# Kernel tuning notes

Measured on AMD Instinct MI355X. Metric: run time of the kernel, lower is better.

Reference implementation:

```python
import jax, jax.numpy as jnp
import numpy as np

D = 512          # input_size (feature dim)
C = 100          # num_classes
N = 2048         # test samples
ALPHA = 0.5      # regularization mixing parameter
SHRINK = 1e-4    # shrinkage_param


def setup_inputs() -> dict:
    key = jax.random.key(0)
    k1, k2, k3, k4, k5 = jax.random.split(key, 5)
    X = jax.random.normal(k1, (N, D), dtype=jnp.float32)
    muK = jax.random.normal(k2, (C, D), dtype=jnp.float32)
    # Per-class covariances: PSD, well-conditioned (like fitted streaming covariances)
    A = jax.random.normal(k3, (C, D, D), dtype=jnp.float32) * 0.05
    SigmaK = jnp.einsum('cij,ckj->cik', A, A) + 0.1 * jnp.eye(D, dtype=jnp.float32)
    B = jax.random.normal(k4, (D, D), dtype=jnp.float32) * 0.05
    Sigma = B @ B.T + 0.1 * jnp.eye(D, dtype=jnp.float32)
    # class counts (all > 0 so every class is active)
    cK = jax.random.uniform(k5, (C,), dtype=jnp.float32, minval=1.0, maxval=1000.0)
    return {"X": X, "muK": muK, "SigmaK": SigmaK, "Sigma": Sigma, "cK": cK}


def reference(X, muK, SigmaK, Sigma, cK):
    # RegSigmaK[k] = alpha * SigmaK[k] + (1-alpha) * Sigma           [C, D, D]
    RegSigmaK = ALPHA * SigmaK + (1.0 - ALPHA) * Sigma[None, :, :]
    # priors (classes with zero count get prior 1, then are masked to -inf below)
    s = jnp.sum(cK)
    prior = jnp.where(cK == 0, 1.0, cK / s)                          # [C]
    # Lambda[k] = pinv((1-sh) * RegSigmaK[k] + sh * I)               [C, D, D]
    eye = jnp.eye(D, dtype=RegSigmaK.dtype)
    Lambda = jnp.linalg.pinv((1.0 - SHRINK) * RegSigmaK + SHRINK * eye)
    # 0.5 * log ||RegSigmaK[k]||_F  (torch.norm default = Frobenius)
    half_lognorm = 0.5 * jnp.log(jnp.linalg.norm(RegSigmaK, axis=(1, 2)))  # [C]
    # batched Mahalanobis quadratic form: (x - mu_k)^T Lambda_k (x - mu_k)
    diff = X[:, None, :] - muK[None, :, :]                           # [N, C, D]
    quad = jnp.einsum('ncd,cde,nce->nc', diff, Lambda, diff)         # [N, C]
    scores = jnp.log(prior)[None, :] - half_lognorm[None, :] - 0.5 * quad
    scores = jnp.where((cK == 0)[None, :], -jnp.inf, scores)
    return scores
```

## Files before the change

kernel.cpp:

```cpp
#include <hip/hip_runtime.h>
#include <math.h>

#define DIM 512
#define NCLS 100
#define NS 2048
#define DD (DIM*DIM)
#define SHRINKV 1e-4f

typedef short bf16x8 __attribute__((ext_vector_type(8)));
typedef short s16x4 __attribute__((ext_vector_type(4)));
typedef float f32x4 __attribute__((ext_vector_type(4)));

static __device__ __forceinline__ short f2bf(float f) {
  unsigned int u = __float_as_uint(f);
  u += 0x7FFFu + ((u >> 16) & 1u);
  return (short)(u >> 16);
}

__global__ void aux_kernel(const float* __restrict__ cK, float* __restrict__ aux) {
  __shared__ float red[128];
  int t = threadIdx.x;
  float v = (t < NCLS) ? cK[t] : 0.f;
  if (t < NCLS) aux[1 + t] = 0.f;
  red[t] = v;
  __syncthreads();
  for (int o = 64; o > 0; o >>= 1) {
    if (t < o) red[t] += red[t + o];
    __syncthreads();
  }
  if (t == 0) aux[0] = red[0];
}

__global__ __launch_bounds__(256) void prep_kernel(const float* __restrict__ SigmaK,
                                                   const float* __restrict__ Sigma,
                                                   float* __restrict__ M,
                                                   float* __restrict__ aux) {
  int b = blockIdx.x;
  int k = b >> 2, chunk = b & 3;
  const float* Sk = SigmaK + (size_t)k * DD;
  float* Mk = M + (size_t)k * DD;
  int base0 = chunk << 16;
  float fro = 0.f;
  const float oms = 1.0f - SHRINKV;
  for (int it = 0; it < 64; ++it) {
    int idx = base0 + (it << 10) + (threadIdx.x << 2);
    float4 a = *(const float4*)(Sk + idx);
    float4 g = *(const float4*)(Sigma + idx);
    int r = idx >> 9, c = idx & 511;
    float4 reg;
    reg.x = 0.5f*(a.x + g.x); reg.y = 0.5f*(a.y + g.y);
    reg.z = 0.5f*(a.z + g.z); reg.w = 0.5f*(a.w + g.w);
    fro += reg.x*reg.x + reg.y*reg.y + reg.z*reg.z + reg.w*reg.w;
    float4 m;
    m.x = oms*reg.x + ((r == c + 0) ? SHRINKV : 0.f);
    m.y = oms*reg.y + ((r == c + 1) ? SHRINKV : 0.f);
    m.z = oms*reg.z + ((r == c + 2) ? SHRINKV : 0.f);
    m.w = oms*reg.w + ((r == c + 3) ? SHRINKV : 0.f);
    *(float4*)(Mk + idx) = m;
  }
  __shared__ float red[4];
  int lane = threadIdx.x & 63, w = threadIdx.x >> 6;
  for (int o = 32; o > 0; o >>= 1) fro += __shfl_down(fro, o);
  if (lane == 0) red[w] = fro;
  __syncthreads();
  if (threadIdx.x == 0) atomicAdd(&aux[1 + k], red[0] + red[1] + red[2] + red[3]);
}

__global__ __launch_bounds__(64) void fdiag_kernel(float* __restrict__ M,
                                                   short* __restrict__ Wb, int p) {
  __shared__ float Llds[64 * 68];
  int kcls = blockIdx.x;
  int lane = threadIdx.x;
  int p0 = p << 6;
  float* Mk = M + (size_t)kcls * DD;
  short* Wk = Wb + (size_t)kcls * DD;
  float row[64];
  {
    const float* src = Mk + (size_t)(p0 + lane) * DIM + p0;
    #pragma unroll
    for (int c4 = 0; c4 < 64; c4 += 4) {
      float4 v = *(const float4*)(src + c4);
      row[c4] = v.x; row[c4+1] = v.y; row[c4+2] = v.z; row[c4+3] = v.w;
    }
  }
  #pragma unroll
  for (int j = 0; j < 64; ++j) {
    float diagv = __shfl(row[j], j);
    float dv = sqrtf(diagv);
    float rinv = 1.0f / dv;
    float myLj = row[j] * rinv;
    row[j] = myLj;
    #pragma unroll
    for (int c = j + 1; c < 64; ++c)
      row[c] = fmaf(-myLj, __shfl(myLj, c), row[c]);
  }
  #pragma unroll
  for (int c = 0; c < 64; ++c)
    Llds[lane * 68 + c] = (c <= lane) ? row[c] : 0.f;
  __syncthreads();
  float w[64];
  #pragma unroll
  for (int r = 0; r < 64; ++r) {
    float s = 0.f;
    #pragma unroll
    for (int kk = 0; kk + 4 <= r; kk += 4) {
      float4 lv = *(const float4*)(Llds + r*68 + kk);
      s += lv.x*w[kk] + lv.y*w[kk+1] + lv.z*w[kk+2] + lv.w*w[kk+3];
    }
    #pragma unroll
    for (int kk = r & ~3; kk < r; ++kk) s += Llds[r*68 + kk] * w[kk];
    float rhs = ((r == lane) ? 1.0f : 0.0f) - s;
    w[r] = rhs / Llds[r*68 + r];
  }
  #pragma unroll
  for (int r = 0; r < 64; ++r) {
    Mk[(size_t)(p0 + r)*DIM + p0 + lane] = w[r];
    Wk[(size_t)(p0 + r)*DIM + p0 + lane] = f2bf(w[r]);
  }
}

__global__ __launch_bounds__(256) void trsm_kernel(float* __restrict__ M, int p) {
  __shared__ float TA[64 * 68];
  __shared__ float TB[64 * 68];
  int n = 7 - p;
  int cls = blockIdx.x / n;
  int bi = blockIdx.x % n;
  int i = p + 1 + bi;
  float* Mk = M + (size_t)cls * DD;
  int tid = threadIdx.x;
  int ty = tid >> 4, tx = tid & 15;
  int sr = tid >> 2, sq = (tid & 3) << 4;
  {
    const float* a = Mk + (size_t)((i << 6) + sr)*DIM + (p << 6) + sq;
    const float* b = Mk + (size_t)((p << 6) + sr)*DIM + (p << 6) + sq;
    #pragma unroll
    for (int t4 = 0; t4 < 4; ++t4) {
      float4 va = *(const float4*)(a + 4*t4);
      TA[(sq+4*t4+0)*68+sr]=va.x; TA[(sq+4*t4+1)*68+sr]=va.y;
      TA[(sq+4*t4+2)*68+sr]=va.z; TA[(sq+4*t4+3)*68+sr]=va.w;
      float4 vb = *(const float4*)(b + 4*t4);
      TB[(sq+4*t4+0)*68+sr]=vb.x; TB[(sq+4*t4+1)*68+sr]=vb.y;
      TB[(sq+4*t4+2)*68+sr]=vb.z; TB[(sq+4*t4+3)*68+sr]=vb.w;
    }
  }
  __syncthreads();
  float acc[4][4];
  #pragma unroll
  for (int a = 0; a < 4; ++a)
    #pragma unroll
    for (int b = 0; b < 4; ++b) acc[a][b] = 0.f;
  #pragma unroll 16
  for (int m = 0; m < 64; ++m) {
    float4 av = *(const float4*)(TA + m*68 + (ty << 2));
    float4 bv = *(const float4*)(TB + m*68 + (tx << 2));
    float a4[4] = {av.x, av.y, av.z, av.w};
    float b4[4] = {bv.x, bv.y, bv.z, bv.w};
    #pragma unroll
    for (int ir = 0; ir < 4; ++ir)
      #pragma unroll
      for (int ic = 0; ic < 4; ++ic) acc[ir][ic] += a4[ir] * b4[ic];
  }
  #pragma unroll
  for (int q = 0; q < 4; ++q) {
    float4 v; v.x = acc[q][0]; v.y = acc[q][1]; v.z = acc[q][2]; v.w = acc[q][3];
    *(float4*)(Mk + (size_t)((i << 6) + (ty << 2) + q)*DIM + (p << 6) + (tx << 2)) = v;
  }
}

__global__ __launch_bounds__(256) void syrk_kernel(float* __restrict__ M, int p) {
  __shared__ float TA[64 * 68];
  __shared__ float TB[64 * 68];
  int n = 7 - p;
  int T = n * (n + 1) / 2;
  int cls = blockIdx.x / T;
  int t = blockIdx.x % T;
  int bi = 0;
  while (t > bi) { t -= bi + 1; ++bi; }
  int i = p + 1 + bi, j = p + 1 + t;
  float* Mk = M + (size_t)cls * DD;
  int tid = threadIdx.x;
  int ty = tid >> 4, tx = tid & 15;
  int sr = tid >> 2, sq = (tid & 3) << 4;
  {
    const float* a = Mk + (size_t)((i << 6) + sr)*DIM + (p << 6) + sq;
    const float* b = Mk + (size_t)((j << 6) + sr)*DIM + (p << 6) + sq;
    #pragma unroll
    for (int t4 = 0; t4 < 4; ++t4) {
      float4 va = *(const float4*)(a + 4*t4);
      TA[(sq+4*t4+0)*68+sr]=va.x; TA[(sq+4*t4+1)*68+sr]=va.y;
      TA[(sq+4*t4+2)*68+sr]=va.z; TA[(sq+4*t4+3)*68+sr]=va.w;
      float4 vb = *(const float4*)(b + 4*t4);
      TB[(sq+4*t4+0)*68+sr]=vb.x; TB[(sq+4*t4+1)*68+sr]=vb.y;
      TB[(sq+4*t4+2)*68+sr]=vb.z; TB[(sq+4*t4+3)*68+sr]=vb.w;
    }
  }
  __syncthreads();
  float acc[4][4];
  #pragma unroll
  for (int a = 0; a < 4; ++a)
    #pragma unroll
    for (int b = 0; b < 4; ++b) acc[a][b] = 0.f;
  #pragma unroll 16
  for (int m = 0; m < 64; ++m) {
    float4 av = *(const float4*)(TA + m*68 + (ty << 2));
    float4 bv = *(const float4*)(TB + m*68 + (tx << 2));
    float a4[4] = {av.x, av.y, av.z, av.w};
    float b4[4] = {bv.x, bv.y, bv.z, bv.w};
    #pragma unroll
    for (int ir = 0; ir < 4; ++ir)
      #pragma unroll
      for (int ic = 0; ic < 4; ++ic) acc[ir][ic] += a4[ir] * b4[ic];
  }
  #pragma unroll
  for (int q = 0; q < 4; ++q) {
    float* dst = Mk + (size_t)((i << 6) + (ty << 2) + q)*DIM + (j << 6) + (tx << 2);
    float4 v = *(const float4*)dst;
    v.x -= acc[q][0]; v.y -= acc[q][1]; v.z -= acc[q][2]; v.w -= acc[q][3];
    *(float4*)dst = v;
  }
}

__global__ __launch_bounds__(256) void sweep_kernel(float* __restrict__ M,
                                                    short* __restrict__ Wb, int i) {
  __shared__ float TL[64 * 68];
  __shared__ float TW[64 * 68];
  int cls = blockIdx.x / i;
  int j = blockIdx.x % i;
  float* Mk = M + (size_t)cls * DD;
  short* Wk = Wb + (size_t)cls * DD;
  int tid = threadIdx.x;
  int ty = tid >> 4, tx = tid & 15;
  int sr = tid >> 2, sq = (tid & 3) << 4;
  float acc[4][4];
  #pragma unroll
  for (int a = 0; a < 4; ++a)
    #pragma unroll
    for (int b = 0; b < 4; ++b) acc[a][b] = 0.f;
  for (int k = j; k < i; ++k) {
    __syncthreads();
    {
      const float* a = Mk + (size_t)((i << 6) + sr)*DIM + (k << 6) + sq;
      const float* b = Mk + (size_t)((j << 6) + sr)*DIM + (k << 6) + sq;
      #pragma unroll
      for (int t4 = 0; t4 < 4; ++t4) {
        float4 va = *(const float4*)(a + 4*t4);
        TL[(sq+4*t4+0)*68+sr]=va.x; TL[(sq+4*t4+1)*68+sr]=va.y;
        TL[(sq+4*t4+2)*68+sr]=va.z; TL[(sq+4*t4+3)*68+sr]=va.w;
        *(float4*)(TW + sr*68 + sq + 4*t4) = *(const float4*)(b + 4*t4);
      }
    }
    __syncthreads();
    #pragma unroll 16
    for (int m = 0; m < 64; ++m) {
      float4 av = *(const float4*)(TL + m*68 + (ty << 2));
      float4 bv = *(const float4*)(TW + m*68 + (tx << 2));
      float a4[4] = {av.x, av.y, av.z, av.w};
      float b4[4] = {bv.x, bv.y, bv.z, bv.w};
      #pragma unroll
      for (int ir = 0; ir < 4; ++ir)
        #pragma unroll
        for (int ic = 0; ic < 4; ++ic) acc[ir][ic] += a4[ir] * b4[ic];
    }
  }
  __syncthreads();
  #pragma unroll
  for (int q = 0; q < 4; ++q) {
    float4 v; v.x = acc[q][0]; v.y = acc[q][1]; v.z = acc[q][2]; v.w = acc[q][3];
    *(float4*)(TW + ((ty << 2) + q)*68 + (tx << 2)) = v;
  }
  {
    const float* a = Mk + (size_t)((i << 6) + sr)*DIM + (i << 6) + sq;
    #pragma unroll
    for (int t4 = 0; t4 < 4; ++t4) {
      float4 va = *(const float4*)(a + 4*t4);
      TL[(sq+4*t4+0)*68+sr]=va.x; TL[(sq+4*t4+1)*68+sr]=va.y;
      TL[(sq+4*t4+2)*68+sr]=va.z; TL[(sq+4*t4+3)*68+sr]=va.w;
    }
  }
  __syncthreads();
  float r2[4][4];
  #pragma unroll
  for (int a = 0; a < 4; ++a)
    #pragma unroll
    for (int b = 0; b < 4; ++b) r2[a][b] = 0.f;
  #pragma unroll 16
  for (int m = 0; m < 64; ++m) {
    float4 av = *(const float4*)(TL + m*68 + (ty << 2));
    float4 bv = *(const float4*)(TW + m*68 + (tx << 2));
    float a4[4] = {av.x, av.y, av.z, av.w};
    float b4[4] = {bv.x, bv.y, bv.z, bv.w};
    #pragma unroll
    for (int ir = 0; ir < 4; ++ir)
      #pragma unroll
      for (int ic = 0; ic < 4; ++ic) r2[ir][ic] += a4[ir] * b4[ic];
  }
  #pragma unroll
  for (int q = 0; q < 4; ++q) {
    int a = (ty << 2) + q;
    float4 v; v.x = -r2[q][0]; v.y = -r2[q][1]; v.z = -r2[q][2]; v.w = -r2[q][3];
    *(float4*)(Mk + (size_t)((j << 6) + a)*DIM + (i << 6) + (tx << 2)) = v;
    s16x4 h;
    h[0] = f2bf(v.x); h[1] = f2bf(v.y); h[2] = f2bf(v.z); h[3] = f2bf(v.w);
    *(s16x4*)(Wk + (size_t)((i << 6) + a)*DIM + (j << 6) + (tx << 2)) = h;
  }
}

__global__ __launch_bounds__(256) void score_kernel(const float* __restrict__ X,
                                                    const float* __restrict__ muK,
                                                    const float* __restrict__ cK,
                                                    const short* __restrict__ W,
                                                    const float* __restrict__ aux,
                                                    float* __restrict__ out) {
  __shared__ __align__(16) short diffB[64 * 64];
  __shared__ __align__(16) short WB[64 * 64];
  int bid = blockIdx.x;
  int kc = bid >> 5;
  int n0 = (bid & 31) << 6;
  int tid = threadIdx.x;
  int lane = tid & 63, wv = tid >> 6;
  int srow = tid >> 2;
  int sc4 = (tid & 3) << 4;
  const short* Wk = W + (size_t)kc * DD;
  const float* mu = muK + (size_t)kc * DIM;

  f32x4 acc[8][4];
  #pragma unroll
  for (int a = 0; a < 8; ++a)
    #pragma unroll
    for (int b = 0; b < 4; ++b) { acc[a][b][0]=0.f; acc[a][b][1]=0.f; acc[a][b][2]=0.f; acc[a][b][3]=0.f; }

  int sb0 = ((srow << 7) + (sc4 << 1)) ^ ((srow & 7) << 4);
  int sb1 = ((srow << 7) + (sc4 << 1) + 16) ^ ((srow & 7) << 4);

  #pragma unroll
  for (int dc = 0; dc < 8; ++dc) {
    __syncthreads();
    {
      const float* xr = X + (size_t)(n0 + srow)*DIM + (dc << 6) + sc4;
      const float* mr = mu + (dc << 6) + sc4;
      float4 x0 = *(const float4*)(xr + 0);
      float4 x1 = *(const float4*)(xr + 4);
      float4 x2 = *(const float4*)(xr + 8);
      float4 x3 = *(const float4*)(xr + 12);
      float4 m0 = *(const float4*)(mr + 0);
      float4 m1 = *(const float4*)(mr + 4);
      float4 m2 = *(const float4*)(mr + 8);
      float4 m3 = *(const float4*)(mr + 12);
      bf16x8 h0, h1;
      h0[0]=f2bf(x0.x-m0.x); h0[1]=f2bf(x0.y-m0.y); h0[2]=f2bf(x0.z-m0.z); h0[3]=f2bf(x0.w-m0.w);
      h0[4]=f2bf(x1.x-m1.x); h0[5]=f2bf(x1.y-m1.y); h0[6]=f2bf(x1.z-m1.z); h0[7]=f2bf(x1.w-m1.w);
      h1[0]=f2bf(x2.x-m2.x); h1[1]=f2bf(x2.y-m2.y); h1[2]=f2bf(x2.z-m2.z); h1[3]=f2bf(x2.w-m2.w);
      h1[4]=f2bf(x3.x-m3.x); h1[5]=f2bf(x3.y-m3.y); h1[6]=f2bf(x3.z-m3.z); h1[7]=f2bf(x3.w-m3.w);
      *(bf16x8*)((char*)diffB + sb0) = h0;
      *(bf16x8*)((char*)diffB + sb1) = h1;
    }
    #pragma unroll
    for (int jt = dc; jt < 8; ++jt) {
      __syncthreads();
      {
        const short* wr = Wk + (size_t)((jt << 6) + srow)*DIM + (dc << 6) + sc4;
        uint4 wa = *(const uint4*)(wr);
        uint4 wb2 = *(const uint4*)(wr + 8);
        *(uint4*)((char*)WB + sb0) = wa;
        *(uint4*)((char*)WB + sb1) = wb2;
      }
      __syncthreads();
      int r16 = lane & 15;
      int k8 = (lane >> 4) << 3;
      int arow = (wv << 4) + r16;
      #pragma unroll
      for (int ks = 0; ks < 2; ++ks) {
        bf16x8 af = *(const bf16x8*)((const char*)diffB +
                     (((arow << 7) + (((ks << 5) + k8) << 1)) ^ ((arow & 7) << 4)));
        #pragma unroll
        for (int jj = 0; jj < 4; ++jj) {
          int brow = (jj << 4) + r16;
          bf16x8 bfr = *(const bf16x8*)((const char*)WB +
                       (((brow << 7) + (((ks << 5) + k8) << 1)) ^ ((brow & 7) << 4)));
          acc[jt][jj] = __builtin_amdgcn_mfma_f32_16x16x32_bf16(af, bfr, acc[jt][jj], 0, 0, 0);
        }
      }
    }
  }
  float qp[4] = {0.f, 0.f, 0.f, 0.f};
  #pragma unroll
  for (int jt2 = 0; jt2 < 8; ++jt2)
    #pragma unroll
    for (int jj = 0; jj < 4; ++jj)
      #pragma unroll
      for (int r = 0; r < 4; ++r) { float y = acc[jt2][jj][r]; qp[r] += y * y; }
  #pragma unroll
  for (int r = 0; r < 4; ++r) {
    qp[r] += __shfl_xor(qp[r], 1);
    qp[r] += __shfl_xor(qp[r], 2);
    qp[r] += __shfl_xor(qp[r], 4);
    qp[r] += __shfl_xor(qp[r], 8);
  }
  float ck = cK[kc];
  float base;
  if (ck == 0.f) base = -INFINITY;
  else base = logf(ck) - logf(aux[0]) - 0.25f * logf(aux[1 + kc]);
  if ((lane & 15) == 0) {
    int nbase = n0 + (wv << 4) + ((lane >> 4) << 2);
    #pragma unroll
    for (int r = 0; r < 4; ++r)
      out[(size_t)(nbase + r)*NCLS + kc] = base - 0.5f * qp[r];
  }
}

extern "C" void kernel_launch(void* const* d_in, const int* in_sizes, int n_in,
                              void* d_out, int out_size, void* d_ws, size_t ws_size,
                              hipStream_t stream) {
  (void)in_sizes; (void)n_in; (void)out_size; (void)ws_size;
  const float* X      = (const float*)d_in[0];
  const float* muK    = (const float*)d_in[1];
  const float* SigmaK = (const float*)d_in[2];
  const float* Sigma  = (const float*)d_in[3];
  const float* cK     = (const float*)d_in[4];
  float* out = (float*)d_out;
  char* ws = (char*)d_ws;
  float* M   = (float*)ws;
  short* W   = (short*)(ws + (size_t)NCLS * DD * 4);
  float* aux = (float*)(ws + (size_t)NCLS * DD * 6);

  aux_kernel<<<1, 128, 0, stream>>>(cK, aux);
  prep_kernel<<<400, 256, 0, stream>>>(SigmaK, Sigma, M, aux);
  for (int p = 0; p < 8; ++p) {
    fdiag_kernel<<<NCLS, 64, 0, stream>>>(M, W, p);
    int n = 7 - p;
    if (n > 0) {
      trsm_kernel<<<NCLS * n, 256, 0, stream>>>(M, p);
      syrk_kernel<<<NCLS * (n * (n + 1) / 2), 256, 0, stream>>>(M, p);
    }
  }
  for (int i = 1; i < 8; ++i)
    sweep_kernel<<<NCLS * i, 256, 0, stream>>>(M, W, i);
  score_kernel<<<NCLS * 32, 256, 0, stream>>>(X, muK, cK, W, aux, out);
}
```

Measured before the change: 909.4 us.

## Fuse Cholesky diag+trsm, merge tail steps, double-buffer score kernel W tiles

```diff
diff --git a/kernel.cpp b/kernel.cpp
--- a/kernel.cpp
+++ b/kernel.cpp
@@ -15,20 +15,6 @@
   unsigned int u = __float_as_uint(f);
   u += 0x7FFFu + ((u >> 16) & 1u);
   return (short)(u >> 16);
-}
-
-__global__ void aux_kernel(const float* __restrict__ cK, float* __restrict__ aux) {
-  __shared__ float red[128];
-  int t = threadIdx.x;
-  float v = (t < NCLS) ? cK[t] : 0.f;
-  if (t < NCLS) aux[1 + t] = 0.f;
-  red[t] = v;
-  __syncthreads();
-  for (int o = 64; o > 0; o >>= 1) {
-    if (t < o) red[t] += red[t + o];
-    __syncthreads();
-  }
-  if (t == 0) aux[0] = red[0];
 }
 
 __global__ __launch_bounds__(256) void prep_kernel(const float* __restrict__ SigmaK,
@@ -66,104 +52,98 @@
   if (threadIdx.x == 0) atomicAdd(&aux[1 + k], red[0] + red[1] + red[2] + red[3]);
 }
 
-__global__ __launch_bounds__(64) void fdiag_kernel(float* __restrict__ M,
-                                                   short* __restrict__ Wb, int p) {
+__global__ __launch_bounds__(256) void fdt_kernel(float* __restrict__ M,
+                                                  short* __restrict__ Wb, int p) {
   __shared__ float Llds[64 * 68];
+  __shared__ float invT[64 * 68];
+  __shared__ float TA[64 * 68];
   int kcls = blockIdx.x;
-  int lane = threadIdx.x;
-  int p0 = p << 6;
   float* Mk = M + (size_t)kcls * DD;
   short* Wk = Wb + (size_t)kcls * DD;
-  float row[64];
-  {
+  int tid = threadIdx.x, lane = tid & 63, wv = tid >> 6;
+  int ty = tid >> 4, tx = tid & 15;
+  int sr = tid >> 2, sq = (tid & 3) << 4;
+  int p0 = p << 6;
+  if (wv == 0) {
+    float row[64];
     const float* src = Mk + (size_t)(p0 + lane) * DIM + p0;
     #pragma unroll
     for (int c4 = 0; c4 < 64; c4 += 4) {
       float4 v = *(const float4*)(src + c4);
       row[c4] = v.x; row[c4+1] = v.y; row[c4+2] = v.z; row[c4+3] = v.w;
     }
-  }
-  #pragma unroll
-  for (int j = 0; j < 64; ++j) {
-    float diagv = __shfl(row[j], j);
-    float dv = sqrtf(diagv);
-    float rinv = 1.0f / dv;
-    float myLj = row[j] * rinv;
-    row[j] = myLj;
-    #pragma unroll
-    for (int c = j + 1; c < 64; ++c)
-      row[c] = fmaf(-myLj, __shfl(myLj, c), row[c]);
-  }
-  #pragma unroll
-  for (int c = 0; c < 64; ++c)
-    Llds[lane * 68 + c] = (c <= lane) ? row[c] : 0.f;
-  __syncthreads();
-  float w[64];
-  #pragma unroll
-  for (int r = 0; r < 64; ++r) {
-    float s = 0.f;
-    #pragma unroll
-    for (int kk = 0; kk + 4 <= r; kk += 4) {
-      float4 lv = *(const float4*)(Llds + r*68 + kk);
-      s += lv.x*w[kk] + lv.y*w[kk+1] + lv.z*w[kk+2] + lv.w*w[kk+3];
-    }
-    #pragma unroll
-    for (int kk = r & ~3; kk < r; ++kk) s += Llds[r*68 + kk] * w[kk];
-    float rhs = ((r == lane) ? 1.0f : 0.0f) - s;
-    w[r] = rhs / Llds[r*68 + r];
-  }
-  #pragma unroll
-  for (int r = 0; r < 64; ++r) {
-    Mk[(size_t)(p0 + r)*DIM + p0 + lane] = w[r];
-    Wk[(size_t)(p0 + r)*DIM + p0 + lane] = f2bf(w[r]);
-  }
-}
-
-__global__ __launch_bounds__(256) void trsm_kernel(float* __restrict__ M, int p) {
-  __shared__ float TA[64 * 68];
-  __shared__ float TB[64 * 68];
-  int n = 7 - p;
-  int cls = blockIdx.x / n;
-  int bi = blockIdx.x % n;
-  int i = p + 1 + bi;
-  float* Mk = M + (size_t)cls * DD;
-  int tid = threadIdx.x;
-  int ty = tid >> 4, tx = tid & 15;
-  int sr = tid >> 2, sq = (tid & 3) << 4;
-  {
-    const float* a = Mk + (size_t)((i << 6) + sr)*DIM + (p << 6) + sq;
-    const float* b = Mk + (size_t)((p << 6) + sr)*DIM + (p << 6) + sq;
-    #pragma unroll
-    for (int t4 = 0; t4 < 4; ++t4) {
-      float4 va = *(const float4*)(a + 4*t4);
-      TA[(sq+4*t4+0)*68+sr]=va.x; TA[(sq+4*t4+1)*68+sr]=va.y;
-      TA[(sq+4*t4+2)*68+sr]=va.z; TA[(sq+4*t4+3)*68+sr]=va.w;
-      float4 vb = *(const float4*)(b + 4*t4);
-      TB[(sq+4*t4+0)*68+sr]=vb.x; TB[(sq+4*t4+1)*68+sr]=vb.y;
-      TB[(sq+4*t4+2)*68+sr]=vb.z; TB[(sq+4*t4+3)*68+sr]=vb.w;
-    }
-  }
-  __syncthreads();
-  float acc[4][4];
-  #pragma unroll
-  for (int a = 0; a < 4; ++a)
-    #pragma unroll
-    for (int b = 0; b < 4; ++b) acc[a][b] = 0.f;
-  #pragma unroll 16
-  for (int m = 0; m < 64; ++m) {
-    float4 av = *(const float4*)(TA + m*68 + (ty << 2));
-    float4 bv = *(const float4*)(TB + m*68 + (tx << 2));
-    float a4[4] = {av.x, av.y, av.z, av.w};
-    float b4[4] = {bv.x, bv.y, bv.z, bv.w};
-    #pragma unroll
-    for (int ir = 0; ir < 4; ++ir)
-      #pragma unroll
-      for (int ic = 0; ic < 4; ++ic) acc[ir][ic] += a4[ir] * b4[ic];
-  }
-  #pragma unroll
-  for (int q = 0; q < 4; ++q) {
-    float4 v; v.x = acc[q][0]; v.y = acc[q][1]; v.z = acc[q][2]; v.w = acc[q][3];
-    *(float4*)(Mk + (size_t)((i << 6) + (ty << 2) + q)*DIM + (p << 6) + (tx << 2)) = v;
+    #pragma unroll
+    for (int j = 0; j < 64; ++j) {
+      float diagv = __shfl(row[j], j);
+      float dv = sqrtf(diagv);
+      float rinv = 1.0f / dv;
+      float myLj = row[j] * rinv;
+      row[j] = myLj;
+      #pragma unroll
+      for (int c = j + 1; c < 64; ++c)
+        row[c] = fmaf(-myLj, __shfl(myLj, c), row[c]);
+    }
+    #pragma unroll
+    for (int c = 0; c < 64; ++c)
+      Llds[lane * 68 + c] = (c <= lane) ? row[c] : 0.f;
+  }
+  __syncthreads();
+  if (wv == 0) {
+    float w[64];
+    #pragma unroll
+    for (int r = 0; r < 64; ++r) {
+      float s = 0.f;
+      #pragma unroll
+      for (int kk = 0; kk + 4 <= r; kk += 4) {
+        float4 lv = *(const float4*)(Llds + r*68 + kk);
+        s += lv.x*w[kk] + lv.y*w[kk+1] + lv.z*w[kk+2] + lv.w*w[kk+3];
+      }
+      #pragma unroll
+      for (int kk = r & ~3; kk < r; ++kk) s += Llds[r*68 + kk] * w[kk];
+      float rhs = ((r == lane) ? 1.0f : 0.0f) - s;
+      w[r] = rhs / Llds[r*68 + r];
+    }
+    #pragma unroll
+    for (int r = 0; r < 64; ++r) {
+      Mk[(size_t)(p0 + r)*DIM + p0 + lane] = w[r];
+      Wk[(size_t)(p0 + r)*DIM + p0 + lane] = f2bf(w[r]);
+      invT[lane*68 + r] = w[r];
+    }
+  }
+  __syncthreads();
+  for (int i = p + 1; i < 8; ++i) {
+    {
+      const float* a = Mk + (size_t)((i << 6) + sr)*DIM + p0 + sq;
+      #pragma unroll
+      for (int t4 = 0; t4 < 4; ++t4) {
+        float4 va = *(const float4*)(a + 4*t4);
+        TA[(sq+4*t4+0)*68+sr]=va.x; TA[(sq+4*t4+1)*68+sr]=va.y;
+        TA[(sq+4*t4+2)*68+sr]=va.z; TA[(sq+4*t4+3)*68+sr]=va.w;
+      }
+    }
+    __syncthreads();
+    float acc[4][4];
+    #pragma unroll
+    for (int a2 = 0; a2 < 4; ++a2)
+      #pragma unroll
+      for (int b2 = 0; b2 < 4; ++b2) acc[a2][b2] = 0.f;
+    #pragma unroll 16
+    for (int m = 0; m < 64; ++m) {
+      float4 av = *(const float4*)(TA + m*68 + (ty << 2));
+      float4 bv = *(const float4*)(invT + m*68 + (tx << 2));
+      float a4[4] = {av.x, av.y, av.z, av.w};
+      float b4[4] = {bv.x, bv.y, bv.z, bv.w};
+      #pragma unroll
+      for (int ir = 0; ir < 4; ++ir)
+        #pragma unroll
+        for (int ic = 0; ic < 4; ++ic) acc[ir][ic] += a4[ir] * b4[ic];
+    }
+    #pragma unroll
+    for (int q = 0; q < 4; ++q) {
+      float4 v; v.x = acc[q][0]; v.y = acc[q][1]; v.z = acc[q][2]; v.w = acc[q][3];
+      *(float4*)(Mk + (size_t)((i << 6) + (ty << 2) + q)*DIM + p0 + (tx << 2)) = v;
+    }
+    __syncthreads();
   }
 }
 
@@ -220,6 +200,147 @@
   }
 }
 
+__global__ __launch_bounds__(256) void tail_kernel(float* __restrict__ M,
+                                                   short* __restrict__ Wb) {
+  __shared__ float Llds[64 * 68];
+  __shared__ float invT[64 * 68];
+  __shared__ float TA[64 * 68];
+  __shared__ float TB[64 * 68];
+  int kcls = blockIdx.x;
+  float* Mk = M + (size_t)kcls * DD;
+  short* Wk = Wb + (size_t)kcls * DD;
+  int tid = threadIdx.x, lane = tid & 63, wv = tid >> 6;
+  int ty = tid >> 4, tx = tid & 15;
+  int sr = tid >> 2, sq = (tid & 3) << 4;
+  for (int p = 4; p < 8; ++p) {
+    int p0 = p << 6;
+    __syncthreads();
+    if (wv == 0) {
+      float row[64];
+      const float* src = Mk + (size_t)(p0 + lane) * DIM + p0;
+      #pragma unroll
+      for (int c4 = 0; c4 < 64; c4 += 4) {
+        float4 v = *(const float4*)(src + c4);
+        row[c4] = v.x; row[c4+1] = v.y; row[c4+2] = v.z; row[c4+3] = v.w;
+      }
+      #pragma unroll
+      for (int j = 0; j < 64; ++j) {
+        float diagv = __shfl(row[j], j);
+        float dv = sqrtf(diagv);
+        float rinv = 1.0f / dv;
+        float myLj = row[j] * rinv;
+        row[j] = myLj;
+        #pragma unroll
+        for (int c = j + 1; c < 64; ++c)
+          row[c] = fmaf(-myLj, __shfl(myLj, c), row[c]);
+      }
+      #pragma unroll
+      for (int c = 0; c < 64; ++c)
+        Llds[lane * 68 + c] = (c <= lane) ? row[c] : 0.f;
+    }
+    __syncthreads();
+    if (wv == 0) {
+      float w[64];
+      #pragma unroll
+      for (int r = 0; r < 64; ++r) {
+        float s = 0.f;
+        #pragma unroll
+        for (int kk = 0; kk + 4 <= r; kk += 4) {
+          float4 lv = *(const float4*)(Llds + r*68 + kk);
+          s += lv.x*w[kk] + lv.y*w[kk+1] + lv.z*w[kk+2] + lv.w*w[kk+3];
+        }
+        #pragma unroll
+        for (int kk = r & ~3; kk < r; ++kk) s += Llds[r*68 + kk] * w[kk];
+        float rhs = ((r == lane) ? 1.0f : 0.0f) - s;
+        w[r] = rhs / Llds[r*68 + r];
+      }
+      #pragma unroll
+      for (int r = 0; r < 64; ++r) {
+        Mk[(size_t)(p0 + r)*DIM + p0 + lane] = w[r];
+        Wk[(size_t)(p0 + r)*DIM + p0 + lane] = f2bf(w[r]);
+        invT[lane*68 + r] = w[r];
+      }
+    }
+    __syncthreads();
+    for (int i = p + 1; i < 8; ++i) {
+      {
+        const float* a = Mk + (size_t)((i << 6) + sr)*DIM + p0 + sq;
+        #pragma unroll
+        for (int t4 = 0; t4 < 4; ++t4) {
+          float4 va = *(const float4*)(a + 4*t4);
+          TA[(sq+4*t4+0)*68+sr]=va.x; TA[(sq+4*t4+1)*68+sr]=va.y;
+          TA[(sq+4*t4+2)*68+sr]=va.z; TA[(sq+4*t4+3)*68+sr]=va.w;
+        }
+      }
+      __syncthreads();
+      float acc[4][4];
+      #pragma unroll
+      for (int a2 = 0; a2 < 4; ++a2)
+        #pragma unroll
+        for (int b2 = 0; b2 < 4; ++b2) acc[a2][b2] = 0.f;
+      #pragma unroll 16
+      for (int m = 0; m < 64; ++m) {
+        float4 av = *(const float4*)(TA + m*68 + (ty << 2));
+        float4 bv = *(const float4*)(invT + m*68 + (tx << 2));
+        float a4[4] = {av.x, av.y, av.z, av.w};
+        float b4[4] = {bv.x, bv.y, bv.z, bv.w};
+        #pragma unroll
+        for (int ir = 0; ir < 4; ++ir)
+          #pragma unroll
+          for (int ic = 0; ic < 4; ++ic) acc[ir][ic] += a4[ir] * b4[ic];
+      }
+      #pragma unroll
+      for (int q = 0; q < 4; ++q) {
+        float4 v; v.x = acc[q][0]; v.y = acc[q][1]; v.z = acc[q][2]; v.w = acc[q][3];
+        *(float4*)(Mk + (size_t)((i << 6) + (ty << 2) + q)*DIM + p0 + (tx << 2)) = v;
+      }
+      __syncthreads();
+    }
+    for (int i = p + 1; i < 8; ++i) {
+      for (int j = p + 1; j <= i; ++j) {
+        {
+          const float* a = Mk + (size_t)((i << 6) + sr)*DIM + p0 + sq;
+          const float* b = Mk + (size_t)((j << 6) + sr)*DIM + p0 + sq;
+          #pragma unroll
+          for (int t4 = 0; t4 < 4; ++t4) {
+            float4 va = *(const float4*)(a + 4*t4);
+            TA[(sq+4*t4+0)*68+sr]=va.x; TA[(sq+4*t4+1)*68+sr]=va.y;
+            TA[(sq+4*t4+2)*68+sr]=va.z; TA[(sq+4*t4+3)*68+sr]=va.w;
+            float4 vb = *(const float4*)(b + 4*t4);
+            TB[(sq+4*t4+0)*68+sr]=vb.x; TB[(sq+4*t4+1)*68+sr]=vb.y;
+            TB[(sq+4*t4+2)*68+sr]=vb.z; TB[(sq+4*t4+3)*68+sr]=vb.w;
+          }
+        }
+        __syncthreads();
+        float acc[4][4];
+        #pragma unroll
+        for (int a2 = 0; a2 < 4; ++a2)
+          #pragma unroll
+          for (int b2 = 0; b2 < 4; ++b2) acc[a2][b2] = 0.f;
+        #pragma unroll 16
+        for (int m = 0; m < 64; ++m) {
+          float4 av = *(const float4*)(TA + m*68 + (ty << 2));
+          float4 bv = *(const float4*)(TB + m*68 + (tx << 2));
+          float a4[4] = {av.x, av.y, av.z, av.w};
+          float b4[4] = {bv.x, bv.y, bv.z, bv.w};
+          #pragma unroll
+          for (int ir = 0; ir < 4; ++ir)
+            #pragma unroll
+            for (int ic = 0; ic < 4; ++ic) acc[ir][ic] += a4[ir] * b4[ic];
+        }
+        #pragma unroll
+        for (int q = 0; q < 4; ++q) {
+          float* dst = Mk + (size_t)((i << 6) + (ty << 2) + q)*DIM + (j << 6) + (tx << 2);
+          float4 v = *(const float4*)dst;
+          v.x -= acc[q][0]; v.y -= acc[q][1]; v.z -= acc[q][2]; v.w -= acc[q][3];
+          *(float4*)dst = v;
+        }
+        __syncthreads();
+      }
+    }
+  }
+}
+
 __global__ __launch_bounds__(256) void sweep_kernel(float* __restrict__ M,
                                                     short* __restrict__ Wb, int i) {
   __shared__ float TL[64 * 68];
@@ -305,14 +426,14 @@
   }
 }
 
-__global__ __launch_bounds__(256) void score_kernel(const float* __restrict__ X,
-                                                    const float* __restrict__ muK,
-                                                    const float* __restrict__ cK,
-                                                    const short* __restrict__ W,
-                                                    const float* __restrict__ aux,
-                                                    float* __restrict__ out) {
-  __shared__ __align__(16) short diffB[64 * 64];
-  __shared__ __align__(16) short WB[64 * 64];
+__global__ __launch_bounds__(256, 3) void score_kernel(const float* __restrict__ X,
+                                                       const float* __restrict__ muK,
+                                                       const float* __restrict__ cK,
+                                                       const short* __restrict__ W,
+                                                       const float* __restrict__ aux,
+                                                       float* __restrict__ out) {
+  __shared__ __align__(16) short WBs[2][4096];
+  __shared__ float sred[4];
   int bid = blockIdx.x;
   int kc = bid >> 5;
   int n0 = (bid & 31) << 6;
@@ -322,73 +443,91 @@
   int sc4 = (tid & 3) << 4;
   const short* Wk = W + (size_t)kc * DD;
   const float* mu = muK + (size_t)kc * DIM;
-
-  f32x4 acc[8][4];
-  #pragma unroll
-  for (int a = 0; a < 8; ++a)
-    #pragma unroll
-    for (int b = 0; b < 4; ++b) { acc[a][b][0]=0.f; acc[a][b][1]=0.f; acc[a][b][2]=0.f; acc[a][b][3]=0.f; }
-
+  int r16 = lane & 15;
+  int k8 = (lane >> 4) << 3;
+  int arow = (wv << 4) + r16;
+
+  bf16x8 af[8][2];
+  #pragma unroll
+  for (int dc = 0; dc < 8; ++dc) {
+    #pragma unroll
+    for (int ks = 0; ks < 2; ++ks) {
+      int col = (dc << 6) + (ks << 5) + k8;
+      const float* xp = X + (size_t)(n0 + arow)*DIM + col;
+      float4 x0 = *(const float4*)xp;
+      float4 x1 = *(const float4*)(xp + 4);
+      float4 m0 = *(const float4*)(mu + col);
+      float4 m1 = *(const float4*)(mu + col + 4);
+      bf16x8 h;
+      h[0]=f2bf(x0.x-m0.x); h[1]=f2bf(x0.y-m0.y); h[2]=f2bf(x0.z-m0.z); h[3]=f2bf(x0.w-m0.w);
+      h[4]=f2bf(x1.x-m1.x); h[5]=f2bf(x1.y-m1.y); h[6]=f2bf(x1.z-m1.z); h[7]=f2bf(x1.w-m1.w);
+      af[dc][ks] = h;
+    }
+  }
+  {
+    float v = (tid < NCLS) ? cK[tid] : 0.f;
+    #pragma unroll
+    for (int o = 32; o > 0; o >>= 1) v += __shfl_xor(v, o);
+    if (lane == 0) sred[wv] = v;
+  }
   int sb0 = ((srow << 7) + (sc4 << 1)) ^ ((srow & 7) << 4);
   int sb1 = ((srow << 7) + (sc4 << 1) + 16) ^ ((srow & 7) << 4);
 
-  #pragma unroll
-  for (int dc = 0; dc < 8; ++dc) {
-    __syncthreads();
-    {
-      const float* xr = X + (size_t)(n0 + srow)*DIM + (dc << 6) + sc4;
-      const float* mr = mu + (dc << 6) + sc4;
-      float4 x0 = *(const float4*)(xr + 0);
-      float4 x1 = *(const float4*)(xr + 4);
-      float4 x2 = *(const float4*)(xr + 8);
-      float4 x3 = *(const float4*)(xr + 12);
-      float4 m0 = *(const float4*)(mr + 0);
-      float4 m1 = *(const float4*)(mr + 4);
-      float4 m2 = *(const float4*)(mr + 8);
-      float4 m3 = *(const float4*)(mr + 12);
-      bf16x8 h0, h1;
-      h0[0]=f2bf(x0.x-m0.x); h0[1]=f2bf(x0.y-m0.y); h0[2]=f2bf(x0.z-m0.z); h0[3]=f2bf(x0.w-m0.w);
-      h0[4]=f2bf(x1.x-m1.x); h0[5]=f2bf(x1.y-m1.y); h0[6]=f2bf(x1.z-m1.z); h0[7]=f2bf(x1.w-m1.w);
-      h1[0]=f2bf(x2.x-m2.x); h1[1]=f2bf(x2.y-m2.y); h1[2]=f2bf(x2.z-m2.z); h1[3]=f2bf(x2.w-m2.w);
-      h1[4]=f2bf(x3.x-m3.x); h1[5]=f2bf(x3.y-m3.y); h1[6]=f2bf(x3.z-m3.z); h1[7]=f2bf(x3.w-m3.w);
-      *(bf16x8*)((char*)diffB + sb0) = h0;
-      *(bf16x8*)((char*)diffB + sb1) = h1;
-    }
-    #pragma unroll
-    for (int jt = dc; jt < 8; ++jt) {
-      __syncthreads();
-      {
-        const short* wr = Wk + (size_t)((jt << 6) + srow)*DIM + (dc << 6) + sc4;
-        uint4 wa = *(const uint4*)(wr);
-        uint4 wb2 = *(const uint4*)(wr + 8);
-        *(uint4*)((char*)WB + sb0) = wa;
-        *(uint4*)((char*)WB + sb1) = wb2;
-      }
-      __syncthreads();
-      int r16 = lane & 15;
-      int k8 = (lane >> 4) << 3;
-      int arow = (wv << 4) + r16;
+  uint4 rg[2][2];
+  {
+    const uint4* p0 = (const uint4*)(Wk + (size_t)srow*DIM + sc4);
+    rg[0][0] = p0[0]; rg[0][1] = p0[1];
+  }
+  *(uint4*)((char*)WBs[0] + sb0) = rg[0][0];
+  *(uint4*)((char*)WBs[0] + sb1) = rg[0][1];
+  {
+    const uint4* p1 = (const uint4*)(Wk + (size_t)(64 + srow)*DIM + sc4);
+    rg[1][0] = p1[0]; rg[1][1] = p1[1];
+  }
+  __syncthreads();
+  float sumck = sred[0] + sred[1] + sred[2] + sred[3];
+
+  float qp[4] = {0.f, 0.f, 0.f, 0.f};
+  #pragma unroll
+  for (int jt = 0; jt < 8; ++jt) {
+    f32x4 acc[4];
+    #pragma unroll
+    for (int jj = 0; jj < 4; ++jj) { acc[jj][0]=0.f; acc[jj][1]=0.f; acc[jj][2]=0.f; acc[jj][3]=0.f; }
+    #pragma unroll
+    for (int dc = 0; dc <= jt; ++dc) {
+      const int s = (jt * (jt + 1)) / 2 + dc;
+      const int ns = s + 1;
+      if (ns < 36) {
+        *(uint4*)((char*)WBs[ns & 1] + sb0) = rg[ns & 1][0];
+        *(uint4*)((char*)WBs[ns & 1] + sb1) = rg[ns & 1][1];
+      }
+      if (s + 2 < 36) {
+        int njt = (dc < jt) ? jt : jt + 1;
+        int ndc = (dc < jt) ? dc + 1 : 0;
+        int jt2 = njt, dc2 = ndc + 1;
+        if (dc2 > jt2) { jt2 += 1; dc2 = 0; }
+        const uint4* pp = (const uint4*)(Wk + (size_t)((jt2 << 6) + srow)*DIM + (dc2 << 6) + sc4);
+        rg[s & 1][0] = pp[0]; rg[s & 1][1] = pp[1];
+      }
+      __builtin_amdgcn_s_setprio(1);
       #pragma unroll
       for (int ks = 0; ks < 2; ++ks) {
-        bf16x8 af = *(const bf16x8*)((const char*)diffB +
-                     (((arow << 7) + (((ks << 5) + k8) << 1)) ^ ((arow & 7) << 4)));
         #pragma unroll
         for (int jj = 0; jj < 4; ++jj) {
           int brow = (jj << 4) + r16;
-          bf16x8 bfr = *(const bf16x8*)((const char*)WB +
+          bf16x8 bfr = *(const bf16x8*)((const char*)WBs[s & 1] +
                        (((brow << 7) + (((ks << 5) + k8) << 1)) ^ ((brow & 7) << 4)));
-          acc[jt][jj] = __builtin_amdgcn_mfma_f32_16x16x32_bf16(af, bfr, acc[jt][jj], 0, 0, 0);
+          acc[jj] = __builtin_amdgcn_mfma_f32_16x16x32_bf16(af[dc][ks], bfr, acc[jj], 0, 0, 0);
         }
       }
-    }
-  }
-  float qp[4] = {0.f, 0.f, 0.f, 0.f};
-  #pragma unroll
-  for (int jt2 = 0; jt2 < 8; ++jt2)
+      __builtin_amdgcn_s_setprio(0);
+      __syncthreads();
+    }
     #pragma unroll
     for (int jj = 0; jj < 4; ++jj)
       #pragma unroll
-      for (int r = 0; r < 4; ++r) { float y = acc[jt2][jj][r]; qp[r] += y * y; }
+      for (int r = 0; r < 4; ++r) { float y = acc[jj][r]; qp[r] += y * y; }
+  }
   #pragma unroll
   for (int r = 0; r < 4; ++r) {
     qp[r] += __shfl_xor(qp[r], 1);
@@ -399,7 +538,7 @@
   float ck = cK[kc];
   float base;
   if (ck == 0.f) base = -INFINITY;
-  else base = logf(ck) - logf(aux[0]) - 0.25f * logf(aux[1 + kc]);
+  else base = logf(ck) - logf(sumck) - 0.25f * logf(aux[1 + kc]);
   if ((lane & 15) == 0) {
     int nbase = n0 + (wv << 4) + ((lane >> 4) << 2);
     #pragma unroll
@@ -423,16 +562,14 @@
   short* W   = (short*)(ws + (size_t)NCLS * DD * 4);
   float* aux = (float*)(ws + (size_t)NCLS * DD * 6);
 
-  aux_kernel<<<1, 128, 0, stream>>>(cK, aux);
+  hipMemsetAsync(aux, 0, (1 + NCLS) * sizeof(float), stream);
   prep_kernel<<<400, 256, 0, stream>>>(SigmaK, Sigma, M, aux);
-  for (int p = 0; p < 8; ++p) {
-    fdiag_kernel<<<NCLS, 64, 0, stream>>>(M, W, p);
+  for (int p = 0; p < 4; ++p) {
+    fdt_kernel<<<NCLS, 256, 0, stream>>>(M, W, p);
     int n = 7 - p;
-    if (n > 0) {
-      trsm_kernel<<<NCLS * n, 256, 0, stream>>>(M, p);
-      syrk_kernel<<<NCLS * (n * (n + 1) / 2), 256, 0, stream>>>(M, p);
-    }
-  }
+    syrk_kernel<<<NCLS * (n * (n + 1) / 2), 256, 0, stream>>>(M, p);
+  }
+  tail_kernel<<<NCLS, 256, 0, stream>>>(M, W);
   for (int i = 1; i < 8; ++i)
     sweep_kernel<<<NCLS * i, 256, 0, stream>>>(M, W, i);
   score_kernel<<<NCLS * 32, 256, 0, stream>>>(X, muK, cK, W, aux, out);
```

Measured after the change: 1.202 ms. 32.2% more time.
